# Kernel optimization log

Hardware: AMD Instinct MI355X
Metric: run time of the kernel (lower is better)

Reference implementation:

```python
import jax, jax.numpy as jnp
import numpy as np
import math

D_MODEL = 1024
EXPAND = 2
D_INNER = D_MODEL * EXPAND  # 2048
D_STATE = 16
DT_RANK = max(1, (D_MODEL + 15) // 16)  # 64
K = 4  # conv kernel size
B, S = 2, 2048


def silu(v):
    return v * jax.nn.sigmoid(v)


def setup_inputs() -> dict:
    key = jax.random.key(0)
    ks = jax.random.split(key, 12)
    sc = lambda fan_in: 1.0 / math.sqrt(fan_in)
    x = jax.random.normal(ks[0], (B, S, D_MODEL), dtype=jnp.float32)
    Win = jax.random.normal(ks[1], (D_MODEL, 2 * D_INNER), dtype=jnp.float32) * sc(D_MODEL)
    Wconv = jax.random.normal(ks[2], (D_INNER, 1, K), dtype=jnp.float32) * sc(K)
    bconv = jax.random.normal(ks[3], (D_INNER,), dtype=jnp.float32) * 0.01
    Wx = jax.random.normal(ks[4], (D_INNER, DT_RANK + 2 * D_STATE), dtype=jnp.float32) * sc(D_INNER)
    Wdt = jax.random.normal(ks[5], (DT_RANK, D_INNER), dtype=jnp.float32) * sc(DT_RANK)
    # dt_proj bias init: inverse-softplus of dt ~ LogUniform[1e-3, 1e-1]
    dt = jnp.exp(jax.random.uniform(ks[6], (D_INNER,)) * (math.log(0.1) - math.log(0.001)) + math.log(0.001))
    dt = jnp.clip(dt, 0.0001, None)
    bdt = dt + jnp.log(-jnp.expm1(-dt))
    a = jnp.arange(1, D_STATE + 1, dtype=jnp.float32)[None, :].repeat(D_INNER, axis=0)
    a = a + jax.random.uniform(ks[7], a.shape) * 0.1
    A_log = jnp.log(a)
    Dp = jnp.ones((D_INNER,), dtype=jnp.float32)
    Wout = jax.random.normal(ks[8], (D_INNER, D_MODEL), dtype=jnp.float32) * sc(D_INNER)
    return {"x": x, "Win": Win, "Wconv": Wconv, "bconv": bconv, "Wx": Wx,
            "Wdt": Wdt, "bdt": bdt, "A_log": A_log, "Dp": Dp, "Wout": Wout}


def causal_dw_conv(x, Wconv, bconv):
    # x: [B, S, C] -> depthwise causal conv along S
    xc = jnp.transpose(x, (0, 2, 1))  # [B, C, S]
    y = jax.lax.conv_general_dilated(
        xc, Wconv, window_strides=(1,), padding=[(K - 1, 0)],
        feature_group_count=D_INNER,
        dimension_numbers=("NCH", "OIH", "NCH"))
    y = y + bconv[None, :, None]
    return jnp.transpose(y, (0, 2, 1))  # [B, S, C]


def selective_scan(u, delta, b_term, c_term, A_log, Dp):
    # u, delta: [B,S,Di]; b_term, c_term: [B,S,Ds]
    a = -jnp.exp(A_log)  # [Di, Ds]
    delta_a = jnp.exp(delta[..., None] * a[None, None])            # [B,S,Di,Ds] fp32
    delta_b_u = (delta * u)[..., None] * b_term[:, :, None, :]     # [B,S,Di,Ds]
    du = u * Dp[None, None, :]                                     # [B,S,Di]
    # time-major for scan
    dA = jnp.transpose(delta_a, (1, 0, 2, 3))
    dBu = jnp.transpose(delta_b_u, (1, 0, 2, 3))
    c_t = jnp.transpose(c_term, (1, 0, 2))
    du_t = jnp.transpose(du, (1, 0, 2))

    def step(state, inp):
        dA_t, dBu_t, c, duv = inp
        state = dA_t * state + dBu_t                  # [B,Di,Ds]
        y = jnp.einsum("bdn,bn->bd", state, c) + duv  # [B,Di]
        return state, y

    init = jnp.zeros((u.shape[0], D_INNER, D_STATE), dtype=jnp.float32)
    _, ys = jax.lax.scan(step, init, (dA, dBu, c_t, du_t))
    return jnp.transpose(ys, (1, 0, 2))  # [B,S,Di]


def reference(x, Win, Wconv, bconv, Wx, Wdt, bdt, A_log, Dp, Wout):
    xz = x @ Win                              # [B,S,2*Di]
    x_branch, z_branch = jnp.split(xz, 2, axis=-1)
    x_branch = silu(causal_dw_conv(x_branch, Wconv, bconv))
    params = x_branch @ Wx                    # [B,S,R+2*Ds]
    delta, b_term, c_term = jnp.split(params, [DT_RANK, DT_RANK + D_STATE], axis=-1)
    delta = jax.nn.softplus(delta @ Wdt + bdt)
    y = selective_scan(x_branch, delta, b_term, c_term, A_log, Dp)
    y = y * silu(z_branch)
    return y @ Wout
```

## Files before the change

### kernel.cpp

```cpp
#include <hip/hip_runtime.h>

typedef unsigned short u16;
typedef _Float16 f16;
typedef f16 f16x8 __attribute__((ext_vector_type(8)));
typedef u16 u16x8 __attribute__((ext_vector_type(8)));
typedef short s16x8 __attribute__((ext_vector_type(8)));
typedef float f32x2 __attribute__((ext_vector_type(2)));
typedef float f32x4 __attribute__((ext_vector_type(4)));
typedef float f32x8 __attribute__((ext_vector_type(8)));

#define T_TOK 4096
#define B_SZ 2
#define S_LEN 2048
#define DMODEL 1024
#define DI 2048
#define DS 16
#define RNK 64
#define NCH 64
#define CLEN 32
#define LDXZ 4096
#define SK 8
#define PRM_SLICE (4096 * 128)
#define LOG2E 1.4426950408889634f

#define GLOAD_LDS16(gp, lp)                                                                   \
  __builtin_amdgcn_global_load_lds((const __attribute__((address_space(1))) void*)(gp),       \
                                   (__attribute__((address_space(3))) void*)(lp), 16, 0, 0)

__device__ __forceinline__ float b2f(u16 v) { return __uint_as_float(((unsigned)v) << 16); }
__device__ __forceinline__ u16 f2b(float f) {
  unsigned u = __float_as_uint(f);
  return (u16)((u + 0x7fffu + ((u >> 16) & 1u)) >> 16);
}
__device__ __forceinline__ float fexp2(float x) {
#if __has_builtin(__builtin_amdgcn_exp2f)
  return __builtin_amdgcn_exp2f(x);
#else
  return exp2f(x);
#endif
}
__device__ __forceinline__ int dtype_of(const void* dp) {
  unsigned v = *(const unsigned*)dp;
  return (v == 0x3F800000u) ? 0 : (v == 0x3C003C00u) ? 2 : 1;
}
__device__ __forceinline__ float load_any(const void* p, size_t i, int flag) {
  if (flag == 0) return ((const float*)p)[i];
  if (flag == 1) return b2f(((const u16*)p)[i]);
  return (float)((const f16*)p)[i];
}

__device__ __forceinline__ void tr_tile(const void* __restrict__ src, void* __restrict__ dst,
                                        int R, int C, int Cpad, int f, int bx, int by, int ob) {
  __shared__ f16 t[32][33];
  int c0 = bx * 32, r0 = by * 32;
  int tx = threadIdx.x & 31, ty = threadIdx.x >> 5;
#pragma unroll
  for (int i = ty; i < 32; i += 8) {
    int r = r0 + i, c = c0 + tx;
    float v = (r < R && c < C) ? load_any(src, (size_t)r * C + c, f) : 0.f;
    t[i][tx] = (f16)v;
  }
  __syncthreads();
#pragma unroll
  for (int i = ty; i < 32; i += 8) {
    int c = c0 + i, r = r0 + tx;
    if (c < Cpad && r < R) {
      if (ob) ((u16*)dst)[(size_t)c * R + r] = f2b((float)t[tx][i]);
      else ((f16*)dst)[(size_t)c * R + r] = t[tx][i];
    }
  }
}

__global__ __launch_bounds__(256) void k_prep(const void* __restrict__ Wconv, const void* __restrict__ bconv,
                                              const void* __restrict__ bdt, const void* __restrict__ A_log,
                                              const void* __restrict__ Dp, const void* __restrict__ Wx,
                                              const void* __restrict__ Wdt, const void* __restrict__ Win,
                                              const void* __restrict__ x, f16* __restrict__ WxT,
                                              f16* __restrict__ WdtT, u16* __restrict__ WinTb,
                                              u16* __restrict__ xhb, float* __restrict__ a_f,
                                              float* __restrict__ wconv_f, float* __restrict__ bconv_f,
                                              float* __restrict__ bdt_f, float* __restrict__ dp_f,
                                              int* __restrict__ flag) {
  int f = dtype_of(Dp);
  int bid = blockIdx.x, t = threadIdx.x;
  if (bid < 128) {
    int i = bid * 256 + t;
    a_f[i] = -__expf(load_any(A_log, i, f)) * LOG2E;
  } else if (bid < 160) {
    int i = (bid - 128) * 256 + t;
    wconv_f[i] = load_any(Wconv, i, f);
  } else if (bid < 168) {
    int i = (bid - 160) * 256 + t;
    bconv_f[i] = load_any(bconv, i, f);
  } else if (bid < 176) {
    int i = (bid - 168) * 256 + t;
    bdt_f[i] = load_any(bdt, i, f);
  } else if (bid < 184) {
    int i = (bid - 176) * 256 + t;
    dp_f[i] = load_any(Dp, i, f);
  } else if (bid == 184) {
    if (t == 0) *flag = f;
  } else if (bid < 441) {
    int id = bid - 185;
    tr_tile(Wx, WxT, 2048, 96, 128, f, id & 3, id >> 2, 0);
  } else if (bid < 569) {
    int id = bid - 441;
    tr_tile(Wdt, WdtT, 64, 2048, 2048, f, id & 63, id >> 6, 0);
  } else if (bid < 4665) {
    int id = bid - 569;
    tr_tile(Win, WinTb, 1024, 4096, 4096, f, id & 127, id >> 7, 1);
  } else {
    if (f == 1) return;
    size_t i = (size_t)(bid - 4665) * 2048 + (size_t)t * 8;
    u16x8 o;
    if (f == 0) {
      const float* s = (const float*)x + i;
#pragma unroll
      for (int j = 0; j < 8; ++j) o[j] = f2b(s[j]);
    } else {
      const f16* s = (const f16*)x + i;
#pragma unroll
      for (int j = 0; j < 8; ++j) o[j] = f2b((float)s[j]);
    }
    *(u16x8*)(xhb + i) = o;
  }
}

__global__ __launch_bounds__(256) void k_transpose16(const void* __restrict__ src, f16* __restrict__ dst,
                                                     int R, int C, int Cpad, const void* __restrict__ Dp) {
  tr_tile(src, dst, R, C, Cpad, dtype_of(Dp), blockIdx.x, blockIdx.y, 0);
}

__global__ __launch_bounds__(512) void k_gemm1(const void* __restrict__ x0, const u16* __restrict__ xhb,
                                               const u16* __restrict__ Bw, f16* __restrict__ C,
                                               const int* __restrict__ flag) {
  constexpr int LD = 1024, LDC = LDXZ, NT = 16, NP = NT / 2;
  __shared__ __align__(16) u16 lds[8 * 8192];
  const u16* A = (*flag == 1) ? (const u16*)x0 : xhb;
  const int tid = threadIdx.x;
  const int wv = tid >> 6, ln = tid & 63;
  const int quad = ln >> 4, l16 = ln & 15;
  const int wr = wv >> 2, wc = wv & 3;
  const int m0 = blockIdx.y * 256, n0 = blockIdx.x * 256;
  const int rr = tid >> 3;
  const int cc = (tid & 7) ^ (rr & 7);
  const u16* aBase = A + (size_t)m0 * LD + cc * 8;
  const u16* bBase = Bw + (size_t)n0 * LD + cc * 8;
  const int brow = ((tid >> 8) << 6) + (rr & 31);
  u16* const dBase = lds + wv * 512;
  auto stageA = [&](int tile, int mq) {
    const u16* s = aBase + (size_t)(mq * 64 + rr) * LD + tile * 64;
    u16* d = dBase + ((tile & 1) * 4 + mq) * 8192;
    GLOAD_LDS16(s, d);
    GLOAD_LDS16(s + 128 * LD, d + 4096);
  };
  auto stageB = [&](int tile, int nq) {
    const u16* s = bBase + (size_t)(brow + nq * 32) * LD + tile * 64;
    u16* d = dBase + ((tile & 1) * 4 + 2 + nq) * 8192;
    GLOAD_LDS16(s, d);
    GLOAD_LDS16(s + 128 * LD, d + 4096);
  };
  const int rxor = (l16 & 7) << 3;
  f32x4 acc[8][4] = {};
  stageA(0, 0); stageB(0, 1); stageB(0, 0); stageA(0, 1);
  stageA(1, 0); stageB(1, 1);
  asm volatile("s_waitcnt vmcnt(4)" ::: "memory");
  __builtin_amdgcn_s_barrier();
  s16x8 af[4][2], bf[2][2];
  for (int pr = 0; pr < NP; ++pr) {
    const int t0 = 2 * pr;
    const bool more = (pr < NP - 1);
#pragma unroll
    for (int ph = 0; ph < 8; ++ph) {
      const int slot = ph >> 2, q = ph & 3;
      const int mq = q >> 1, nq = (q >> 1) ^ (q & 1);
      const u16* Ar = lds + (slot * 4 + mq) * 8192;
      const u16* Br = lds + (slot * 4 + 2 + nq) * 8192;
      if (q == 0 || q == 2) {
#pragma unroll
        for (int i = 0; i < 4; ++i) {
          const int ra = wr * 64 + i * 16 + l16;
#pragma unroll
          for (int kk = 0; kk < 2; ++kk)
            af[i][kk] = *(const s16x8*)(Ar + ra * 64 + ((kk * 32 + quad * 8) ^ rxor));
        }
      }
      if (q != 2) {
#pragma unroll
        for (int j = 0; j < 2; ++j) {
          const int rb = wc * 32 + j * 16 + l16;
#pragma unroll
          for (int kk = 0; kk < 2; ++kk)
            bf[j][kk] = *(const s16x8*)(Br + rb * 64 + ((kk * 32 + quad * 8) ^ rxor));
        }
      }
      if (ph == 0) stageB(t0 + 1, 0);
      else if (ph == 1) stageA(t0 + 1, 1);
      else if (more) {
        if (ph == 2) stageA(t0 + 2, 0);
        else if (ph == 3) stageB(t0 + 2, 1);
        else if (ph == 4) stageB(t0 + 2, 0);
        else if (ph == 5) stageA(t0 + 2, 1);
        else if (ph == 6) stageA(t0 + 3, 0);
        else stageB(t0 + 3, 1);
      }
      __builtin_amdgcn_s_barrier();
      asm volatile("s_waitcnt lgkmcnt(0)" ::: "memory");
      __builtin_amdgcn_sched_barrier(0);
      __builtin_amdgcn_s_setprio(1);
#pragma unroll
      for (int kk = 0; kk < 2; ++kk)
#pragma unroll
        for (int i = 0; i < 4; ++i)
#pragma unroll
          for (int j = 0; j < 2; ++j)
            acc[mq * 4 + i][nq * 2 + j] = __builtin_amdgcn_mfma_f32_16x16x32_bf16(
                af[i][kk], bf[j][kk], acc[mq * 4 + i][nq * 2 + j], 0, 0, 0);
      __builtin_amdgcn_s_setprio(0);
      if (ph == 3) {
        if (more) asm volatile("s_waitcnt vmcnt(6)" ::: "memory");
        else asm volatile("s_waitcnt vmcnt(2)" ::: "memory");
      } else if (ph == 5) {
        if (more) asm volatile("s_waitcnt vmcnt(8)" ::: "memory");
        else asm volatile("s_waitcnt vmcnt(0)" ::: "memory");
      } else if (ph == 7) {
        if (more) asm volatile("s_waitcnt vmcnt(4)" ::: "memory");
        else asm volatile("s_waitcnt vmcnt(0)" ::: "memory");
      }
      __builtin_amdgcn_s_barrier();
    }
  }
#pragma unroll
  for (int i = 0; i < 8; ++i)
#pragma unroll
    for (int j = 0; j < 4; ++j)
#pragma unroll
      for (int r = 0; r < 4; ++r) {
        const int row = m0 + wr * 128 + i * 16 + quad * 4 + r;
        const int col = n0 + wc * 64 + j * 16 + l16;
        C[(size_t)row * LDC + col] = (f16)acc[i][j][r];
      }
}

template <int BM, int BN, int EPI>
__global__ __launch_bounds__(256) void k_gemm2(const f16* __restrict__ A, const f16* __restrict__ B,
                                               void* __restrict__ Cv, const float* __restrict__ bias,
                                               const int* __restrict__ flag,
                                               int klen, int lda, int ldb, int ldc) {
  constexpr int WM = BM / 2, WN = BN / 2;
  constexpr int FM = WM / 16, FN = WN / 16;
  __shared__ __align__(16) f16 As[2 * BM * 32];
  __shared__ __align__(16) f16 Bs[2 * BN * 32];
  const int tid = threadIdx.x;
  const int wv = tid >> 6, ln = tid & 63;
  const int quad = ln >> 4, l16 = ln & 15;
  const int lrow = ln >> 2, lch = (ln & 3) * 8;
  const int m0 = blockIdx.y * BM, n0 = blockIdx.x * BN;
  const int wm = (wv & 1) * WM, wn = (wv >> 1) * WN;
  const int kbase = blockIdx.z * klen;
  f32x4 acc[FM][FN] = {};
  for (int kk = 0; kk < klen; kk += 64) {
    const int k0 = kbase + kk;
    __syncthreads();
#pragma unroll
    for (int h = 0; h < 2; ++h) {
#pragma unroll
      for (int i = 0; i < BM / 64; ++i) {
        int r0 = wv * (BM / 4) + i * 16;
        GLOAD_LDS16(A + (size_t)(m0 + r0 + lrow) * lda + k0 + h * 32 + lch, As + h * BM * 32 + r0 * 32);
      }
#pragma unroll
      for (int i = 0; i < BN / 64; ++i) {
        int r0 = wv * (BN / 4) + i * 16;
        GLOAD_LDS16(B + (size_t)(n0 + r0 + lrow) * ldb + k0 + h * 32 + lch, Bs + h * BN * 32 + r0 * 32);
      }
    }
    __syncthreads();
#pragma unroll
    for (int h = 0; h < 2; ++h) {
      f16x8 af[FM], bf[FN];
#pragma unroll
      for (int i = 0; i < FM; ++i) af[i] = *(const f16x8*)(As + h * BM * 32 + (wm + i * 16 + l16) * 32 + quad * 8);
#pragma unroll
      for (int j = 0; j < FN; ++j) bf[j] = *(const f16x8*)(Bs + h * BN * 32 + (wn + j * 16 + l16) * 32 + quad * 8);
#pragma unroll
      for (int i = 0; i < FM; ++i)
#pragma unroll
        for (int j = 0; j < FN; ++j)
          acc[i][j] = __builtin_amdgcn_mfma_f32_16x16x32_f16(af[i], bf[j], acc[i][j], 0, 0, 0);
    }
  }
  int dflag = 1;
  if constexpr (EPI == 2) dflag = *flag;
  f16* Cz = (f16*)Cv;
  if constexpr (EPI == 4) Cz = (f16*)Cv + (size_t)blockIdx.z * PRM_SLICE;
#pragma unroll
  for (int i = 0; i < FM; ++i)
#pragma unroll
    for (int j = 0; j < FN; ++j)
#pragma unroll
      for (int r = 0; r < 4; ++r) {
        int row = m0 + wm + i * 16 + quad * 4 + r;
        int col = n0 + wn + j * 16 + l16;
        size_t ci = (size_t)row * ldc + col;
        float v = acc[i][j][r];
        if constexpr (EPI == 3) {
          v += bias[row];
          v = (v > 20.f) ? v : log1pf(__expf(v));
          size_t di2 = ((size_t)(row << 1) + (col >> 11)) * (size_t)LDXZ + (col & 2047);
          Cz[di2] = (f16)v;
        } else if constexpr (EPI == 2) {
          if (dflag == 0) ((float*)Cv)[ci] = v;
          else if (dflag == 1) ((u16*)Cv)[ci] = f2b(v);
          else ((f16*)Cv)[ci] = (f16)v;
        } else {
          Cz[ci] = (f16)v;
        }
      }
}

__global__ __launch_bounds__(256) void k_sum_prm(const f16* __restrict__ parts, f16* __restrict__ prm,
                                                 float* __restrict__ prmBC) {
  size_t i = (size_t)(blockIdx.x * 256 + threadIdx.x) * 8;
  int col0 = (int)(i & 127);
  if (col0 >= 96) return;
  float s[8] = {};
#pragma unroll
  for (int z = 0; z < SK; ++z) {
    f16x8 v = *(const f16x8*)(parts + (size_t)z * PRM_SLICE + i);
#pragma unroll
    for (int j = 0; j < 8; ++j) s[j] += (float)v[j];
  }
  if (col0 < 64) {
    f16x8 o;
#pragma unroll
    for (int j = 0; j < 8; ++j) o[j] = (f16)s[j];
    *(f16x8*)(prm + i) = o;
  } else {
    size_t tok = i >> 7;
    f32x8 of;
#pragma unroll
    for (int j = 0; j < 8; ++j) of[j] = s[j];
    *(f32x8*)(prmBC + tok * 32 + (col0 - 64)) = of;
  }
}

__global__ __launch_bounds__(256) void k_conv_silu(const f16* __restrict__ xz, const float* __restrict__ Wconv,
                                                   const float* __restrict__ bconv, f16* __restrict__ xc) {
  int t = blockIdx.x;
  int s = t & (S_LEN - 1);
  int d8 = threadIdx.x * 8;
  float w[4][8];
#pragma unroll
  for (int i = 0; i < 8; ++i)
#pragma unroll
    for (int j = 0; j < 4; ++j) w[j][i] = Wconv[(d8 + i) * 4 + j];
  float acc[8];
#pragma unroll
  for (int i = 0; i < 8; ++i) acc[i] = bconv[d8 + i];
#pragma unroll
  for (int j = 0; j < 4; ++j) {
    int sl = s - 3 + j;
    if (sl >= 0) {
      f16x8 xv = *(const f16x8*)(xz + (size_t)(t - 3 + j) * LDXZ + d8);
#pragma unroll
      for (int i = 0; i < 8; ++i) acc[i] = fmaf((float)xv[i], w[j][i], acc[i]);
    }
  }
  f16x8 o;
#pragma unroll
  for (int i = 0; i < 8; ++i) {
    float v = acc[i];
    o[i] = (f16)(v / (1.f + __expf(-v)));
  }
  *(f16x8*)(xc + (size_t)t * DI + d8) = o;
}

__global__ __launch_bounds__(256) void k_scan_passA(const f16* __restrict__ dltT, const f16* __restrict__ u,
                                                    const float* __restrict__ prmBC, const float* __restrict__ a_f,
                                                    f16* __restrict__ lcs, float* __restrict__ sumdv) {
  __shared__ __align__(16) f16 u_lds[CLEN][128];
  __shared__ __align__(16) float b_lds[CLEN][16];
  const int tid = threadIdx.x;
  int g = blockIdx.x * 256 + tid;
  int nh = g & 1, p = g >> 1;
  int d = p & (DI - 1);
  int c = (p >> 11) & (NCH - 1);
  int b = p >> 17;
  const int d0 = d & ~127;
  const int t0 = b * S_LEN + c * CLEN;
  {
    const f16* up0 = u + (size_t)t0 * DI + d0;
#pragma unroll
    for (int rep = 0; rep < 2; ++rep) {
      int chunk = rep * 256 + tid;
      int row = chunk >> 4, c16 = chunk & 15;
      *(f16x8*)&u_lds[row][c16 * 8] = *(const f16x8*)(up0 + (size_t)row * DI + c16 * 8);
    }
    const float* bp0 = prmBC + (size_t)t0 * 32;
    int row = tid >> 3, c2 = tid & 7;
    *(f32x2*)&b_lds[row][c2 * 2] = *(const f32x2*)(bp0 + row * 32 + c2 * 2);
  }
  const f16* dp = dltT + (size_t)(2 * d + b) * LDXZ + c * CLEN;
  f16x8 dlv[4];
#pragma unroll
  for (int q = 0; q < 4; ++q) dlv[q] = *(const f16x8*)(dp + q * 8);
  f32x4 a0 = *(const f32x4*)(a_f + d * DS + nh * 8);
  f32x4 a1 = *(const f32x4*)(a_f + d * DS + nh * 8 + 4);
  float a[8] = {a0[0], a0[1], a0[2], a0[3], a1[0], a1[1], a1[2], a1[3]};
  __syncthreads();
  const int dd = d - d0;
  float st[8] = {};
  float sumd = 0.f;
#pragma unroll
  for (int s = 0; s < CLEN; ++s) {
    float dl = (float)dlv[s >> 3][s & 7];
    float uv = (float)u_lds[s][dd];
    f32x4 bv0 = *(const f32x4*)&b_lds[s][nh * 8];
    f32x4 bv1 = *(const f32x4*)&b_lds[s][nh * 8 + 4];
    sumd += dl;
    float dbu = dl * uv;
#pragma unroll
    for (int j = 0; j < 8; ++j) {
      float e = fexp2(dl * a[j]);
      float bj = (j < 4) ? bv0[j & 3] : bv1[j & 3];
      st[j] = fmaf(e, st[j], dbu * bj);
    }
  }
  f16x8 o;
#pragma unroll
  for (int j = 0; j < 8; ++j) o[j] = (f16)st[j];
  *(f16x8*)(lcs + (size_t)p * DS + nh * 8) = o;
  if (nh == 0) sumdv[p] = sumd;
}

__global__ __launch_bounds__(256) void k_scan_passB(f16* __restrict__ lcs, const float* __restrict__ sumdv,
                                                    const float* __restrict__ a_f) {
  int g = blockIdx.x * 256 + threadIdx.x;
  int n = g & 15, d = (g >> 4) & (DI - 1), b = g >> 15;
  float an = a_f[d * DS + n];
  const size_t base = (size_t)b * NCH * DI + d;
  float lf[4], sf[4];
#pragma unroll
  for (int q = 0; q < 4; ++q) {
    size_t pq = base + (size_t)q * DI;
    lf[q] = (float)lcs[pq * DS + n];
    sf[q] = sumdv[pq];
  }
  float init = 0.f;
#pragma unroll
  for (int c = 0; c < NCH; ++c) {
    size_t pc = base + (size_t)c * DI;
    float l = lf[c & 3], sd = sf[c & 3];
    if (c + 4 < NCH) {
      size_t pn = base + (size_t)(c + 4) * DI;
      lf[c & 3] = (float)lcs[pn * DS + n];
      sf[c & 3] = sumdv[pn];
    }
    lcs[pc * DS + n] = (f16)init;
    init = fexp2(sd * an) * init + l;
  }
}

__global__ __launch_bounds__(256) void k_scan_passC(const f16* __restrict__ dltT, const f16* __restrict__ u,
                                                    const float* __restrict__ prmBC, const float* __restrict__ a_f,
                                                    const float* __restrict__ dp_f, const f16* __restrict__ lcs,
                                                    f16* __restrict__ xz) {
  __shared__ __align__(16) f16 u_lds[CLEN][128];
  __shared__ __align__(16) f16 z_lds[CLEN][128];
  __shared__ __align__(16) float bc_lds[CLEN][32];
  const int tid = threadIdx.x;
  int g = blockIdx.x * 256 + tid;
  int nh = g & 1, p = g >> 1;
  int d = p & (DI - 1);
  int c = (p >> 11) & (NCH - 1);
  int b = p >> 17;
  const int d0 = d & ~127;
  const int t0 = b * S_LEN + c * CLEN;
  f16* const zp0 = xz + (size_t)t0 * LDXZ + DI + d0;
  {
    const f16* up0 = u + (size_t)t0 * DI + d0;
#pragma unroll
    for (int rep = 0; rep < 2; ++rep) {
      int chunk = rep * 256 + tid;
      int row = chunk >> 4, c16 = chunk & 15;
      *(f16x8*)&u_lds[row][c16 * 8] = *(const f16x8*)(up0 + (size_t)row * DI + c16 * 8);
      *(f16x8*)&z_lds[row][c16 * 8] = *(const f16x8*)(zp0 + (size_t)row * LDXZ + c16 * 8);
    }
    ((f32x4*)bc_lds)[tid] = ((const f32x4*)(prmBC + (size_t)t0 * 32))[tid];
  }
  const f16* dp = dltT + (size_t)(2 * d + b) * LDXZ + c * CLEN;
  f16x8 dlv[4];
#pragma unroll
  for (int q = 0; q < 4; ++q) dlv[q] = *(const f16x8*)(dp + q * 8);
  f32x4 a0 = *(const f32x4*)(a_f + d * DS + nh * 8);
  f32x4 a1 = *(const f32x4*)(a_f + d * DS + nh * 8 + 4);
  float a[8] = {a0[0], a0[1], a0[2], a0[3], a1[0], a1[1], a1[2], a1[3]};
  float st[8];
  f16x8 iv = *(const f16x8*)(lcs + (size_t)p * DS + nh * 8);
#pragma unroll
  for (int j = 0; j < 8; ++j) st[j] = (float)iv[j];
  float dpv = dp_f[d];
  __syncthreads();
  const int dd = d - d0;
#pragma unroll
  for (int s = 0; s < CLEN; ++s) {
    float dl = (float)dlv[s >> 3][s & 7];
    float uv = (float)u_lds[s][dd];
    float z = (float)z_lds[s][dd];
    f32x4 bv0 = *(const f32x4*)&bc_lds[s][nh * 8];
    f32x4 bv1 = *(const f32x4*)&bc_lds[s][nh * 8 + 4];
    f32x4 cv0 = *(const f32x4*)&bc_lds[s][16 + nh * 8];
    f32x4 cv1 = *(const f32x4*)&bc_lds[s][16 + nh * 8 + 4];
    float dbu = dl * uv;
    float part = (nh == 0) ? uv * dpv : 0.f;
#pragma unroll
    for (int j = 0; j < 8; ++j) {
      float e = fexp2(dl * a[j]);
      float bj = (j < 4) ? bv0[j & 3] : bv1[j & 3];
      float cj = (j < 4) ? cv0[j & 3] : cv1[j & 3];
      st[j] = fmaf(e, st[j], dbu * bj);
      part = fmaf(st[j], cj, part);
    }
    part += __shfl_xor(part, 1, 64);
    if (nh == 0) {
      float sg = 1.f / (1.f + __expf(-z));
      z_lds[s][dd] = (f16)(part * z * sg);
    }
  }
  __syncthreads();
#pragma unroll
  for (int rep = 0; rep < 2; ++rep) {
    int chunk = rep * 256 + tid;
    int row = chunk >> 4, c16 = chunk & 15;
    *(f16x8*)(zp0 + (size_t)row * LDXZ + c16 * 8) = *(const f16x8*)&z_lds[row][c16 * 8];
  }
}

extern "C" void kernel_launch(void* const* d_in, const int* in_sizes, int n_in,
                              void* d_out, int out_size, void* d_ws, size_t ws_size,
                              hipStream_t stream) {
  const void* x = d_in[0];
  const void* Win = d_in[1];
  const void* Wconv = d_in[2];
  const void* bconv = d_in[3];
  const void* Wx = d_in[4];
  const void* Wdt = d_in[5];
  const void* bdt = d_in[6];
  const void* A_log = d_in[7];
  const void* Dp = d_in[8];
  const void* Wout = d_in[9];
  (void)in_sizes; (void)n_in; (void)out_size; (void)ws_size;

  const size_t KB = 1024, MB = 1024 * 1024;
  char* ws = (char*)d_ws;
  f16* xzh = (f16*)ws;
  u16* xhb = (u16*)(ws + 32 * MB);
  f16* xch = (f16*)(ws + 32 * MB);
  u16* WinTb = (u16*)(ws + 48 * MB);
  f16* parts = (f16*)(ws + 48 * MB);
  f16* lcs = (f16*)(ws + 48 * MB);
  f16* WoutT = (f16*)(ws + 48 * MB);
  float* sumd = (float*)(ws + 56 * MB);
  f16* prm = (f16*)(ws + 57 * MB);
  float* prmBC = (float*)(ws + 58 * MB);
  f16* WxT = (f16*)(ws + 58 * MB + 512 * KB);
  f16* WdtT = (f16*)(ws + 59 * MB);
  float* a_f = (float*)(ws + 59 * MB + 256 * KB);
  float* wconv_f = (float*)(ws + 59 * MB + 384 * KB);
  float* bconv_f = (float*)(ws + 59 * MB + 416 * KB);
  float* bdt_f = (float*)(ws + 59 * MB + 424 * KB);
  float* dp_f = (float*)(ws + 59 * MB + 432 * KB);
  int* flag = (int*)(ws + 59 * MB + 440 * KB);

  k_prep<<<6713, 256, 0, stream>>>(Wconv, bconv, bdt, A_log, Dp, Wx, Wdt, Win, x,
                                   WxT, WdtT, WinTb, xhb, a_f, wconv_f, bconv_f, bdt_f, dp_f, flag);

  k_gemm1<<<dim3(16, 16), 512, 0, stream>>>(x, xhb, WinTb, xzh, flag);
  k_conv_silu<<<T_TOK, 256, 0, stream>>>(xzh, wconv_f, bconv_f, xch);
  k_gemm2<64, 128, 4><<<dim3(1, 4096 / 64, SK), 256, 0, stream>>>(
      xch, WxT, parts, nullptr, flag, 2048 / SK, 2048, 2048, 128);
  k_sum_prm<<<PRM_SLICE / 8 / 256, 256, 0, stream>>>(parts, prm, prmBC);
  k_gemm2<128, 128, 3><<<dim3(4096 / 128, 2048 / 128), 256, 0, stream>>>(
      WdtT, prm, xzh, bdt_f, flag, 64, 64, 128, 0);
  k_scan_passA<<<(B_SZ * NCH * DI * 2) / 256, 256, 0, stream>>>(xzh, xch, prmBC, a_f, lcs, sumd);
  k_scan_passB<<<(B_SZ * DI * DS) / 256, 256, 0, stream>>>(lcs, sumd, a_f);
  k_scan_passC<<<(B_SZ * NCH * DI * 2) / 256, 256, 0, stream>>>(xzh, xch, prmBC, a_f, dp_f, lcs, xzh);
  k_transpose16<<<dim3(1024 / 32, 2048 / 32), 256, 0, stream>>>(Wout, WoutT, 2048, 1024, 1024, Dp);
  k_gemm2<64, 128, 2><<<dim3(1024 / 128, 4096 / 64), 256, 0, stream>>>(
      xzh + DI, WoutT, d_out, nullptr, flag, 2048, LDXZ, 2048, 1024);
}
```

Baseline: 324.4 us.

## Swizzle GEMM LDS layout and split-K the output projection

An XOR swizzle is applied to the 16-byte chunk index in the k_gemm2 shared-memory tiles, on both the global-to-LDS load side and the MFMA fragment read side. This is meant to reduce LDS bank conflicts in every k_gemm2 instance. The final Wout GEMM is also split into four K-slices that write f16 partials into a new workspace region. A new reduction kernel sums them into the output dtype. The split raises block count and parallelism but adds extra partial-sum memory traffic, f16 rounding of the partials, and a dependence on the workspace extending past 64 MB.

After: 330.8 us. No clear change (+2.0%).

```diff
diff --git a/kernel.cpp b/kernel.cpp
--- a/kernel.cpp
+++ b/kernel.cpp
@@ -20,7 +20,9 @@
 #define CLEN 32
 #define LDXZ 4096
 #define SK 8
+#define SK4 4
 #define PRM_SLICE (4096 * 128)
+#define OUT_SLICE (4096 * 1024)
 #define LOG2E 1.4426950408889634f
 
 #define GLOAD_LDS16(gp, lp)                                                                   \
@@ -254,10 +256,12 @@
   const int tid = threadIdx.x;
   const int wv = tid >> 6, ln = tid & 63;
   const int quad = ln >> 4, l16 = ln & 15;
-  const int lrow = ln >> 2, lch = (ln & 3) * 8;
+  const int lrow = ln >> 2;
+  const int lch = (((ln & 3) ^ ((ln >> 3) & 3))) * 8;
   const int m0 = blockIdx.y * BM, n0 = blockIdx.x * BN;
   const int wm = (wv & 1) * WM, wn = (wv >> 1) * WN;
   const int kbase = blockIdx.z * klen;
+  const int qsw = (quad ^ ((l16 >> 1) & 3)) * 8;
   f32x4 acc[FM][FN] = {};
   for (int kk = 0; kk < klen; kk += 64) {
     const int k0 = kbase + kk;
@@ -280,9 +284,9 @@
     for (int h = 0; h < 2; ++h) {
       f16x8 af[FM], bf[FN];
 #pragma unroll
-      for (int i = 0; i < FM; ++i) af[i] = *(const f16x8*)(As + h * BM * 32 + (wm + i * 16 + l16) * 32 + quad * 8);
-#pragma unroll
-      for (int j = 0; j < FN; ++j) bf[j] = *(const f16x8*)(Bs + h * BN * 32 + (wn + j * 16 + l16) * 32 + quad * 8);
+      for (int i = 0; i < FM; ++i) af[i] = *(const f16x8*)(As + h * BM * 32 + (wm + i * 16 + l16) * 32 + qsw);
+#pragma unroll
+      for (int j = 0; j < FN; ++j) bf[j] = *(const f16x8*)(Bs + h * BN * 32 + (wn + j * 16 + l16) * 32 + qsw);
 #pragma unroll
       for (int i = 0; i < FM; ++i)
 #pragma unroll
@@ -294,6 +298,7 @@
   if constexpr (EPI == 2) dflag = *flag;
   f16* Cz = (f16*)Cv;
   if constexpr (EPI == 4) Cz = (f16*)Cv + (size_t)blockIdx.z * PRM_SLICE;
+  if constexpr (EPI == 5) Cz = (f16*)Cv + (size_t)blockIdx.z * OUT_SLICE;
 #pragma unroll
   for (int i = 0; i < FM; ++i)
 #pragma unroll
@@ -342,6 +347,35 @@
 #pragma unroll
     for (int j = 0; j < 8; ++j) of[j] = s[j];
     *(f32x8*)(prmBC + tok * 32 + (col0 - 64)) = of;
+  }
+}
+
+__global__ __launch_bounds__(256) void k_sum_out(const f16* __restrict__ parts, void* __restrict__ out,
+                                                 const int* __restrict__ flag) {
+  size_t i = (size_t)(blockIdx.x * 256 + threadIdx.x) * 8;
+  float s[8] = {};
+#pragma unroll
+  for (int z = 0; z < SK4; ++z) {
+    f16x8 v = *(const f16x8*)(parts + (size_t)z * OUT_SLICE + i);
+#pragma unroll
+    for (int j = 0; j < 8; ++j) s[j] += (float)v[j];
+  }
+  int f = *flag;
+  if (f == 0) {
+    f32x8 o;
+#pragma unroll
+    for (int j = 0; j < 8; ++j) o[j] = s[j];
+    *(f32x8*)((float*)out + i) = o;
+  } else if (f == 1) {
+    u16x8 o;
+#pragma unroll
+    for (int j = 0; j < 8; ++j) o[j] = f2b(s[j]);
+    *(u16x8*)((u16*)out + i) = o;
+  } else {
+    f16x8 o;
+#pragma unroll
+    for (int j = 0; j < 8; ++j) o[j] = (f16)s[j];
+    *(f16x8*)((f16*)out + i) = o;
   }
 }
 
@@ -572,6 +606,7 @@
   float* bdt_f = (float*)(ws + 59 * MB + 424 * KB);
   float* dp_f = (float*)(ws + 59 * MB + 432 * KB);
   int* flag = (int*)(ws + 59 * MB + 440 * KB);
+  f16* parts4 = (f16*)(ws + 64 * MB);
 
   k_prep<<<6713, 256, 0, stream>>>(Wconv, bconv, bdt, A_log, Dp, Wx, Wdt, Win, x,
                                    WxT, WdtT, WinTb, xhb, a_f, wconv_f, bconv_f, bdt_f, dp_f, flag);
@@ -587,6 +622,7 @@
   k_scan_passB<<<(B_SZ * DI * DS) / 256, 256, 0, stream>>>(lcs, sumd, a_f);
   k_scan_passC<<<(B_SZ * NCH * DI * 2) / 256, 256, 0, stream>>>(xzh, xch, prmBC, a_f, dp_f, lcs, xzh);
   k_transpose16<<<dim3(1024 / 32, 2048 / 32), 256, 0, stream>>>(Wout, WoutT, 2048, 1024, 1024, Dp);
-  k_gemm2<64, 128, 2><<<dim3(1024 / 128, 4096 / 64), 256, 0, stream>>>(
-      xzh + DI, WoutT, d_out, nullptr, flag, 2048, LDXZ, 2048, 1024);
-}
+  k_gemm2<64, 128, 5><<<dim3(1024 / 128, 4096 / 64, SK4), 256, 0, stream>>>(
+      xzh + DI, WoutT, parts4, nullptr, flag, 2048 / SK4, LDXZ, 2048, 1024);
+  k_sum_out<<<OUT_SLICE / 8 / 256, 256, 0, stream>>>(parts4, d_out, flag);
+}
```
